# Performance work log

Measured on AMD Instinct MI355X. Metric: run time of the kernel, lower is better.

Reference implementation:

```python
import jax, jax.numpy as jnp
from jax import lax
import numpy as np

D_MODEL = 1024
EXP = 2
D_INNER = EXP * D_MODEL
D_STATE = 16
D_CONV = 4
DT_RANK = 64  # ceil(d_model/16), mamba default
NUM_GROUPS = 4
BSZ, SEQ = 2, 2048
EPS = 1e-5


def setup_inputs() -> dict:
    key = jax.random.key(0)
    ks = jax.random.split(key, 10)
    def n(k, shape, s=0.02):
        return jax.random.normal(k, shape, jnp.float32) * s
    return dict(
        x=jax.random.normal(ks[0], (BSZ, SEQ, D_MODEL), jnp.float32),
        ln1_g=jnp.ones((D_MODEL,), jnp.float32), ln1_b=jnp.zeros((D_MODEL,), jnp.float32),
        ln2_g=jnp.ones((D_MODEL,), jnp.float32), ln2_b=jnp.zeros((D_MODEL,), jnp.float32),
        W1=n(ks[1], (EXP * D_MODEL, D_MODEL)), b1=jnp.zeros((EXP * D_MODEL,), jnp.float32),
        W2=n(ks[2], (D_MODEL, EXP * D_MODEL)), b2=jnp.zeros((D_MODEL,), jnp.float32),
        in_proj_w=n(ks[3], (2 * D_INNER, D_MODEL)),
        conv_w=n(ks[4], (D_INNER, 1, D_CONV), 0.2), conv_b=jnp.zeros((D_INNER,), jnp.float32),
        x_proj_w=n(ks[5], (DT_RANK + 2 * D_STATE, D_INNER)),
        dt_proj_w=n(ks[6], (D_INNER, DT_RANK), 0.1), dt_proj_b=n(ks[7], (D_INNER,), 0.5),
        A_log=jnp.tile(jnp.log(jnp.arange(1, D_STATE + 1, dtype=jnp.float32)), (D_INNER, 1)),
        D_param=jnp.ones((D_INNER,), jnp.float32),
        out_proj_w=n(ks[8], (D_MODEL, D_INNER)),
    )


def _layernorm(x, g, b):
    m = jnp.mean(x, -1, keepdims=True)
    v = jnp.var(x, -1, keepdims=True)
    return (x - m) * lax.rsqrt(v + EPS) * g + b


def _ste_sign(w):
    # sign quantization with straight-through estimator (groupwise split is a no-op for sign)
    return w + lax.stop_gradient(jnp.sign(w) - w)


def _quant_act_groupwise(x, b=8):
    # groups along seq dim (x.shape[1]); gamma is the abs-max over the whole group slab
    Qb = float(2 ** (b - 1))
    B_, L, D = x.shape
    g = x.reshape(B_, NUM_GROUPS, L // NUM_GROUPS, D)
    gamma = jnp.max(jnp.abs(g), axis=(0, 2, 3), keepdims=True)
    q = jnp.clip(g * Qb / (gamma + EPS), -Qb + EPS, Qb - EPS)
    return q.reshape(B_, L, D)


def _mamba(u, in_proj_w, conv_w, conv_b, x_proj_w, dt_proj_w, dt_proj_b, A_log, D_param, out_proj_w):
    B_, L, _ = u.shape
    xz = u @ in_proj_w.T                         # [B, L, 2*d_inner]
    xs, z = jnp.split(xz, 2, axis=-1)
    # depthwise causal conv1d
    xt = jnp.transpose(xs, (0, 2, 1))            # [B, d_inner, L]
    xt = lax.conv_general_dilated(xt, conv_w, (1,), [(D_CONV - 1, 0)],
                                  feature_group_count=D_INNER,
                                  dimension_numbers=('NCH', 'OIH', 'NCH'))
    xt = xt + conv_b[None, :, None]
    xs = jax.nn.silu(jnp.transpose(xt, (0, 2, 1)))  # [B, L, d_inner]
    x_dbl = xs @ x_proj_w.T                      # [B, L, dt_rank + 2*d_state]
    dt, Bm, Cm = jnp.split(x_dbl, [DT_RANK, DT_RANK + D_STATE], axis=-1)
    dt = jax.nn.softplus(dt @ dt_proj_w.T + dt_proj_b)   # [B, L, d_inner]
    A = -jnp.exp(A_log)                          # [d_inner, d_state]

    def step(h, inp):
        dt_s, B_s, C_s, x_s = inp                # [B,di], [B,ds], [B,ds], [B,di]
        dA = jnp.exp(dt_s[..., None] * A)        # [B, di, ds]
        h = h * dA + (dt_s * x_s)[..., None] * B_s[:, None, :]
        y = jnp.einsum('bds,bs->bd', h, C_s)
        return h, y

    tm = lambda a: jnp.transpose(a, (1, 0, 2))   # time-major
    h0 = jnp.zeros((B_, D_INNER, D_STATE), u.dtype)
    _, ys = lax.scan(step, h0, (tm(dt), tm(Bm), tm(Cm), tm(xs)))
    y = jnp.transpose(ys, (1, 0, 2)) + D_param * xs
    y = y * jax.nn.silu(z)
    return y @ out_proj_w.T


def reference(x, ln1_g, ln1_b, ln2_g, ln2_b, W1, b1, W2, b2,
              in_proj_w, conv_w, conv_b, x_proj_w, dt_proj_w, dt_proj_b,
              A_log, D_param, out_proj_w):
    qW1 = _ste_sign(W1)
    qW2 = _ste_sign(W2)
    gated = jnp.clip(_layernorm(x, ln1_g, ln1_b) @ qW1.T + b1, -1.0, 1.0)  # Hardtanh
    x = x + gated @ qW2.T + b2
    qx = _quant_act_groupwise(x)
    out = qx + _mamba(_layernorm(qx, ln2_g, ln2_b), in_proj_w, conv_w, conv_b,
                      x_proj_w, dt_proj_w, dt_proj_b, A_log, D_param, out_proj_w)
    return out
```

## Files before the change

kernel.cpp:

```cpp
#include <hip/hip_runtime.h>
#include <math.h>

#define D_MODEL 1024
#define D_INNER 2048
#define D_STATE 16
#define DT_RANK 64
#define BSZ 2
#define SEQ 2048
#define NTOK (BSZ*SEQ)
#define NCH  (BSZ*D_INNER)
#define NCHUNK 64
#define CLEN 32
#define EPS 1e-5f

typedef __attribute__((ext_vector_type(8))) short short8v;
typedef __attribute__((ext_vector_type(4))) float f32x4;

__device__ __forceinline__ float sgnf(float w) {
    return (w > 0.f) ? 1.f : ((w < 0.f) ? -1.f : 0.f);
}
__device__ __forceinline__ unsigned short f2bf(float f) {
    unsigned int x = __float_as_uint(f);
    x += 0x7fffu + ((x >> 16) & 1u);
    return (unsigned short)(x >> 16);
}
__device__ __forceinline__ float bf2f(unsigned short u) {
    return __uint_as_float(((unsigned int)u) << 16);
}
__device__ __forceinline__ void stage16(const unsigned short* g, unsigned short* l) {
    __builtin_amdgcn_global_load_lds(
        (const __attribute__((address_space(1))) unsigned int*)g,
        (__attribute__((address_space(3))) unsigned int*)l, 16, 0, 0);
}

#define F4_W1   524288
#define F4_C1   524288
#define F4_C2   1048576
#define F4_C3   2097152
#define F4_C4   2146304
#define F4_C5   2179072
#define F4_C6   2703360
__global__ __launch_bounds__(256) void f2bf_all_kernel(
    const float* __restrict__ W1, const float* __restrict__ W2,
    const float* __restrict__ inpj, const float* __restrict__ xpj,
    const float* __restrict__ dtpj, const float* __restrict__ outpj,
    unsigned short* __restrict__ o_w1, unsigned short* __restrict__ o_w2,
    unsigned short* __restrict__ o_in, unsigned short* __restrict__ o_xp,
    unsigned short* __restrict__ o_dt, unsigned short* __restrict__ o_out)
{
    int i = blockIdx.x * 256 + threadIdx.x;
    if (i >= F4_C6) return;
    const float* src; unsigned short* dst; int off; bool sign = false;
    if (i < F4_C1)      { src = W1;   dst = o_w1;  off = i;          sign = true; }
    else if (i < F4_C2) { src = W2;   dst = o_w2;  off = i - F4_C1;  sign = true; }
    else if (i < F4_C3) { src = inpj; dst = o_in;  off = i - F4_C2; }
    else if (i < F4_C4) { src = xpj;  dst = o_xp;  off = i - F4_C3; }
    else if (i < F4_C5) { src = dtpj; dst = o_dt;  off = i - F4_C4; }
    else                { src = outpj;dst = o_out; off = i - F4_C5; }
    float4 v = reinterpret_cast<const float4*>(src)[off];
    if (sign) { v.x = sgnf(v.x); v.y = sgnf(v.y); v.z = sgnf(v.z); v.w = sgnf(v.w); }
    ushort4 o;
    o.x = f2bf(v.x); o.y = f2bf(v.y); o.z = f2bf(v.z); o.w = f2bf(v.w);
    reinterpret_cast<ushort4*>(dst)[off] = o;
}

__global__ __launch_bounds__(256) void ln_hilo_kernel(const float* __restrict__ x,
                                                      const float* __restrict__ g,
                                                      const float* __restrict__ b,
                                                      unsigned short* __restrict__ hi,
                                                      unsigned short* __restrict__ lo) {
    int row = blockIdx.x, tid = threadIdx.x;
    float4 v = reinterpret_cast<const float4*>(x + (size_t)row * D_MODEL)[tid];
    float s = v.x + v.y + v.z + v.w;
    float q = v.x*v.x + v.y*v.y + v.z*v.z + v.w*v.w;
    #pragma unroll
    for (int off = 32; off > 0; off >>= 1) { s += __shfl_down(s, off); q += __shfl_down(q, off); }
    __shared__ float rs[4], rq[4], smean, srstd;
    if ((tid & 63) == 0) { rs[tid >> 6] = s; rq[tid >> 6] = q; }
    __syncthreads();
    if (tid == 0) {
        float ts = rs[0]+rs[1]+rs[2]+rs[3], tq = rq[0]+rq[1]+rq[2]+rq[3];
        float mean = ts * (1.0f / D_MODEL);
        smean = mean;
        srstd = rsqrtf(tq * (1.0f / D_MODEL) - mean*mean + EPS);
    }
    __syncthreads();
    float mean = smean, rstd = srstd;
    float4 gg = reinterpret_cast<const float4*>(g)[tid];
    float4 bb = reinterpret_cast<const float4*>(b)[tid];
    float o[4];
    o[0] = (v.x-mean)*rstd*gg.x + bb.x; o[1] = (v.y-mean)*rstd*gg.y + bb.y;
    o[2] = (v.z-mean)*rstd*gg.z + bb.z; o[3] = (v.w-mean)*rstd*gg.w + bb.w;
    ushort4 h4, l4;
    h4.x = f2bf(o[0]); l4.x = f2bf(o[0] - bf2f(h4.x));
    h4.y = f2bf(o[1]); l4.y = f2bf(o[1] - bf2f(h4.y));
    h4.z = f2bf(o[2]); l4.z = f2bf(o[2] - bf2f(h4.z));
    h4.w = f2bf(o[3]); l4.w = f2bf(o[3] - bf2f(h4.w));
    reinterpret_cast<ushort4*>(hi + (size_t)row * D_MODEL)[tid] = h4;
    reinterpret_cast<ushort4*>(lo + (size_t)row * D_MODEL)[tid] = l4;
}

template<int EP, bool DUALA>
__global__ __launch_bounds__(256) void mfma_gemm(
    const unsigned short* __restrict__ A, const unsigned short* __restrict__ A2,
    const unsigned short* __restrict__ B, float* __restrict__ C,
    unsigned short* __restrict__ Cb,
    int M, int N, int K, int sA, int sC,
    const float* __restrict__ bias, const float* __restrict__ addx, int sAdd,
    unsigned int* __restrict__ gma)
{
    __shared__ __align__(16) unsigned short As[128*32];
    __shared__ __align__(16) unsigned short As2[DUALA ? 128*32 : 8];
    __shared__ __align__(16) unsigned short Bs[128*32];
    __shared__ float redmax[4];
    const int tid = threadIdx.x;
    const int lane = tid & 63;
    const int w = tid >> 6;
    const int wm = w >> 1, wn = w & 1;
    const int row0 = blockIdx.y * 128, col0 = blockIdx.x * 128;
    const int srow = lane >> 2;
    const int scol = (lane & 3) * 8;

    f32x4 acc[4][4];
    #pragma unroll
    for (int m = 0; m < 4; ++m)
        #pragma unroll
        for (int n = 0; n < 4; ++n)
            acc[m][n] = (f32x4){0.f, 0.f, 0.f, 0.f};

    for (int k0 = 0; k0 < K; k0 += 32) {
        #pragma unroll
        for (int i = 0; i < 2; ++i) {
            const int rbase = w * 32 + i * 16;
            stage16(A + (size_t)(row0 + rbase + srow) * sA + k0 + scol, &As[rbase * 32]);
            if (DUALA)
                stage16(A2 + (size_t)(row0 + rbase + srow) * sA + k0 + scol, &As2[rbase * 32]);
            if (col0 + rbase < N)
                stage16(B + (size_t)(col0 + rbase + srow) * K + k0 + scol, &Bs[rbase * 32]);
        }
        __syncthreads();

        short8v af[4], bfr[4], af2[4];
        const int fr = lane & 15, kg = (lane >> 4) * 8;
        #pragma unroll
        for (int m = 0; m < 4; ++m)
            af[m] = *reinterpret_cast<const short8v*>(&As[(wm*64 + m*16 + fr) * 32 + kg]);
        if (DUALA) {
            #pragma unroll
            for (int m = 0; m < 4; ++m)
                af2[m] = *reinterpret_cast<const short8v*>(&As2[(wm*64 + m*16 + fr) * 32 + kg]);
        }
        #pragma unroll
        for (int n = 0; n < 4; ++n)
            bfr[n] = *reinterpret_cast<const short8v*>(&Bs[(wn*64 + n*16 + fr) * 32 + kg]);

        #pragma unroll
        for (int m = 0; m < 4; ++m)
            #pragma unroll
            for (int n = 0; n < 4; ++n) {
                acc[m][n] = __builtin_amdgcn_mfma_f32_16x16x32_bf16(af[m], bfr[n], acc[m][n], 0, 0, 0);
                if (DUALA)
                    acc[m][n] = __builtin_amdgcn_mfma_f32_16x16x32_bf16(af2[m], bfr[n], acc[m][n], 0, 0, 0);
            }
        __syncthreads();
    }

    const int fc = lane & 15, r4 = (lane >> 4) * 4;
    float lmax = 0.0f;
    #pragma unroll
    for (int m = 0; m < 4; ++m) {
        const int grb = row0 + wm*64 + m*16 + r4;
        #pragma unroll
        for (int n = 0; n < 4; ++n) {
            const int gc = col0 + wn*64 + n*16 + fc;
            if (gc >= N) continue;
            #pragma unroll
            for (int j = 0; j < 4; ++j) {
                const int r = grb + j;
                float v = acc[m][n][j];
                if (EP == 0) {
                    C[(size_t)r*sC + gc] = v;
                } else if (EP == 1) {
                    v += bias[gc];
                    v = fminf(1.0f, fmaxf(-1.0f, v));
                    Cb[(size_t)r*sC + gc] = f2bf(v);
                } else if (EP == 3) {
                    float t = v + bias[gc];
                    C[(size_t)r*sC + gc] = fmaxf(t, 0.0f) + log1pf(__expf(-fabsf(t)));
                } else if (EP == 4) {
                    C[(size_t)r*sC + gc] = v + addx[(size_t)r*sAdd + gc];
                } else if (EP == 5) {
                    C[(size_t)r*sC + gc] = v;
                    if (gc < 64) Cb[(size_t)r*64 + gc] = f2bf(v);
                } else if (EP == 6) {
                    Cb[(size_t)r*sC + gc] = f2bf(v);
                } else {
                    v += bias[gc] + addx[(size_t)r*sAdd + gc];
                    C[(size_t)r*sC + gc] = v;
                    lmax = fmaxf(lmax, fabsf(v));
                }
            }
        }
    }
    if (EP == 7) {
        #pragma unroll
        for (int off = 32; off > 0; off >>= 1) lmax = fmaxf(lmax, __shfl_down(lmax, off));
        if (lane == 0) redmax[w] = lmax;
        __syncthreads();
        if (tid == 0) {
            float t = fmaxf(fmaxf(redmax[0], redmax[1]), fmaxf(redmax[2], redmax[3]));
            int g = (row0 & (SEQ - 1)) >> 9;
            atomicMax(gma + g, __float_as_uint(t));
        }
    }
}

__global__ __launch_bounds__(64) void init_gamma_kernel(unsigned int* g) {
    if (threadIdx.x < 4) g[threadIdx.x] = 0u;
}

__global__ __launch_bounds__(256) void quant_ln_kernel(
    const float* __restrict__ x2, const unsigned int* __restrict__ gamma_bits,
    const float* __restrict__ g, const float* __restrict__ b,
    float* __restrict__ qx, unsigned short* __restrict__ u)
{
    int row = blockIdx.x, tid = threadIdx.x;
    int grp = (row & (SEQ - 1)) >> 9;
    float gamma = __uint_as_float(gamma_bits[grp]);
    float scale = 128.0f / (gamma + EPS);
    const float lo = -128.0f + EPS, hi = 128.0f - EPS;
    float4 v = reinterpret_cast<const float4*>(x2 + (size_t)row * D_MODEL)[tid];
    float4 qv;
    qv.x = fminf(hi, fmaxf(lo, v.x * scale));
    qv.y = fminf(hi, fmaxf(lo, v.y * scale));
    qv.z = fminf(hi, fmaxf(lo, v.z * scale));
    qv.w = fminf(hi, fmaxf(lo, v.w * scale));
    reinterpret_cast<float4*>(qx + (size_t)row * D_MODEL)[tid] = qv;
    float s = qv.x + qv.y + qv.z + qv.w;
    float q = qv.x*qv.x + qv.y*qv.y + qv.z*qv.z + qv.w*qv.w;
    #pragma unroll
    for (int off = 32; off > 0; off >>= 1) { s += __shfl_down(s, off); q += __shfl_down(q, off); }
    __shared__ float rs[4], rq[4], smean, srstd;
    if ((tid & 63) == 0) { rs[tid >> 6] = s; rq[tid >> 6] = q; }
    __syncthreads();
    if (tid == 0) {
        float ts = rs[0]+rs[1]+rs[2]+rs[3], tq = rq[0]+rq[1]+rq[2]+rq[3];
        float mean = ts * (1.0f / D_MODEL);
        smean = mean;
        srstd = rsqrtf(tq * (1.0f / D_MODEL) - mean*mean + EPS);
    }
    __syncthreads();
    float mean = smean, rstd = srstd;
    float4 gg = reinterpret_cast<const float4*>(g)[tid];
    float4 bb = reinterpret_cast<const float4*>(b)[tid];
    ushort4 o;
    o.x = f2bf((qv.x-mean)*rstd*gg.x + bb.x);
    o.y = f2bf((qv.y-mean)*rstd*gg.y + bb.y);
    o.z = f2bf((qv.z-mean)*rstd*gg.z + bb.z);
    o.w = f2bf((qv.w-mean)*rstd*gg.w + bb.w);
    reinterpret_cast<ushort4*>(u + (size_t)row * D_MODEL)[tid] = o;
}

__global__ __launch_bounds__(256) void conv_silu_kernel(const unsigned short* __restrict__ xz,
                                                        const float* __restrict__ conv_w,
                                                        const float* __restrict__ conv_b,
                                                        unsigned short* __restrict__ xcb) {
    int c = blockIdx.x * 256 + threadIdx.x;
    int m = blockIdx.y;
    int b = m >> 11, l = m & (SEQ - 1);
    float4 w4 = reinterpret_cast<const float4*>(conv_w)[c];
    float wv[4] = {w4.x, w4.y, w4.z, w4.w};
    float s = conv_b[c];
    const unsigned short* base = xz + ((size_t)b * SEQ) * 4096 + c;
    #pragma unroll
    for (int k = 0; k < 4; ++k) {
        int ll = l - 3 + k;
        if (ll >= 0) s += bf2f(base[(size_t)ll * 4096]) * wv[k];
    }
    float sig = 1.0f / (1.0f + __expf(-s));
    xcb[(size_t)m * D_INNER + c] = f2bf(s * sig);
}

__device__ __forceinline__ void make_dA(float dA[D_STATE], float dtv,
                                        const float* a, bool pw) {
    if (pw) {
        dA[0] = __expf(dtv * a[0]);
        #pragma unroll
        for (int s = 1; s < D_STATE; ++s) dA[s] = dA[s>>1] * dA[(s-1)>>1];
    } else {
        #pragma unroll
        for (int s = 0; s < D_STATE; ++s) dA[s] = __expf(dtv * a[s]);
    }
}

__global__ __launch_bounds__(256) void scan_partial_kernel(
    const float* __restrict__ dt, const unsigned short* __restrict__ xcb,
    const float* __restrict__ xdbl, const float* __restrict__ A_log,
    float* __restrict__ Lbuf, float* __restrict__ Sbuf)
{
    int gtid = blockIdx.x * 256 + threadIdx.x;
    int ch = gtid & (NCH - 1);
    int c  = gtid >> 12;
    int b = ch >> 11, d = ch & (D_INNER - 1);
    float a[D_STATE], h[D_STATE];
    bool pw = true;
    #pragma unroll
    for (int s = 0; s < D_STATE; ++s) {
        a[s] = -__expf(A_log[(size_t)d * D_STATE + s]);
        h[s] = 0.0f;
    }
    #pragma unroll
    for (int s = 1; s < D_STATE; ++s)
        pw = pw && (fabsf(a[s] - a[0]*(float)(s+1)) <= 1e-3f * fabsf(a[s]));

    size_t m0 = (size_t)b * SEQ + (size_t)c * CLEN;
    float Ssum = 0.0f;

    float dt_n = dt[m0 * D_INNER + d];
    float x_n  = bf2f(xcb[m0 * D_INNER + d]);
    float4 B_n[4];
    {
        const float* xd = xdbl + m0 * 96;
        #pragma unroll
        for (int i = 0; i < 4; ++i)
            B_n[i] = *reinterpret_cast<const float4*>(xd + DT_RANK + 4*i);
    }

    for (int l = 0; l < CLEN; ++l) {
        float dtv = dt_n, xv = x_n;
        float Bc[D_STATE];
        #pragma unroll
        for (int i = 0; i < 4; ++i) {
            Bc[4*i+0] = B_n[i].x; Bc[4*i+1] = B_n[i].y; Bc[4*i+2] = B_n[i].z; Bc[4*i+3] = B_n[i].w;
        }
        if (l + 1 < CLEN) {
            size_t m1 = m0 + l + 1;
            dt_n = dt[m1 * D_INNER + d];
            x_n  = bf2f(xcb[m1 * D_INNER + d]);
            const float* xd = xdbl + m1 * 96;
            #pragma unroll
            for (int i = 0; i < 4; ++i)
                B_n[i] = *reinterpret_cast<const float4*>(xd + DT_RANK + 4*i);
        }
        Ssum += dtv;
        float dx = dtv * xv;
        float dA[D_STATE];
        make_dA(dA, dtv, a, pw);
        #pragma unroll
        for (int s = 0; s < D_STATE; ++s)
            h[s] = h[s] * dA[s] + dx * Bc[s];
    }
    float4* Lp = reinterpret_cast<float4*>(Lbuf + (size_t)c * (NCH * D_STATE) + (size_t)ch * D_STATE);
    Lp[0] = make_float4(h[0], h[1], h[2], h[3]);
    Lp[1] = make_float4(h[4], h[5], h[6], h[7]);
    Lp[2] = make_float4(h[8], h[9], h[10], h[11]);
    Lp[3] = make_float4(h[12], h[13], h[14], h[15]);
    Sbuf[(size_t)c * NCH + ch] = Ssum;
}

__global__ __launch_bounds__(256) void scan_combine_kernel(
    float* __restrict__ LH, const float* __restrict__ Sbuf,
    const float* __restrict__ A_log)
{
    int gtid = blockIdx.x * 256 + threadIdx.x;
    int s = gtid & (D_STATE - 1);
    int ch = gtid >> 4;
    int d = ch & (D_INNER - 1);
    float a = -__expf(A_log[(size_t)d * D_STATE + s]);
    float h = 0.0f;
    #pragma unroll 4
    for (int c = 0; c < NCHUNK; ++c) {
        size_t idx = (size_t)c * (NCH * D_STATE) + (size_t)ch * D_STATE + s;
        float loc = LH[idx];
        LH[idx] = h;
        float P = __expf(a * Sbuf[(size_t)c * NCH + ch]);
        h = h * P + loc;
    }
}

__global__ __launch_bounds__(256) void scan_final_kernel(
    const float* __restrict__ dt, const unsigned short* __restrict__ xcb,
    const unsigned short* __restrict__ xzb, const float* __restrict__ xdbl,
    const float* __restrict__ A_log, const float* __restrict__ D_param,
    const float* __restrict__ Hin, unsigned short* __restrict__ yb)
{
    int gtid = blockIdx.x * 256 + threadIdx.x;
    int ch = gtid & (NCH - 1);
    int c  = gtid >> 12;
    int b = ch >> 11, d = ch & (D_INNER - 1);
    float a[D_STATE], h[D_STATE];
    {
        const float4* Hp = reinterpret_cast<const float4*>(
            Hin + (size_t)c * (NCH * D_STATE) + (size_t)ch * D_STATE);
        float4 h0 = Hp[0], h1 = Hp[1], h2 = Hp[2], h3 = Hp[3];
        h[0]=h0.x; h[1]=h0.y; h[2]=h0.z; h[3]=h0.w;
        h[4]=h1.x; h[5]=h1.y; h[6]=h1.z; h[7]=h1.w;
        h[8]=h2.x; h[9]=h2.y; h[10]=h2.z; h[11]=h2.w;
        h[12]=h3.x; h[13]=h3.y; h[14]=h3.z; h[15]=h3.w;
    }
    bool pw = true;
    #pragma unroll
    for (int s = 0; s < D_STATE; ++s)
        a[s] = -__expf(A_log[(size_t)d * D_STATE + s]);
    #pragma unroll
    for (int s = 1; s < D_STATE; ++s)
        pw = pw && (fabsf(a[s] - a[0]*(float)(s+1)) <= 1e-3f * fabsf(a[s]));
    float Dp = D_param[d];

    size_t m0 = (size_t)b * SEQ + (size_t)c * CLEN;
    float dt_n = dt[m0 * D_INNER + d];
    float x_n  = bf2f(xcb[m0 * D_INNER + d]);
    float z_n  = bf2f(xzb[m0 * 4096 + D_INNER + d]);
    float4 B_n[4], C_n[4];
    {
        const float* xd = xdbl + m0 * 96;
        #pragma unroll
        for (int i = 0; i < 4; ++i) {
            B_n[i] = *reinterpret_cast<const float4*>(xd + DT_RANK + 4*i);
            C_n[i] = *reinterpret_cast<const float4*>(xd + DT_RANK + D_STATE + 4*i);
        }
    }

    for (int l = 0; l < CLEN; ++l) {
        float dtv = dt_n, xv = x_n, zv = z_n;
        float Bc[D_STATE], Cc[D_STATE];
        #pragma unroll
        for (int i = 0; i < 4; ++i) {
            Bc[4*i+0] = B_n[i].x; Bc[4*i+1] = B_n[i].y; Bc[4*i+2] = B_n[i].z; Bc[4*i+3] = B_n[i].w;
            Cc[4*i+0] = C_n[i].x; Cc[4*i+1] = C_n[i].y; Cc[4*i+2] = C_n[i].z; Cc[4*i+3] = C_n[i].w;
        }
        if (l + 1 < CLEN) {
            size_t m1 = m0 + l + 1;
            dt_n = dt[m1 * D_INNER + d];
            x_n  = bf2f(xcb[m1 * D_INNER + d]);
            z_n  = bf2f(xzb[m1 * 4096 + D_INNER + d]);
            const float* xd = xdbl + m1 * 96;
            #pragma unroll
            for (int i = 0; i < 4; ++i) {
                B_n[i] = *reinterpret_cast<const float4*>(xd + DT_RANK + 4*i);
                C_n[i] = *reinterpret_cast<const float4*>(xd + DT_RANK + D_STATE + 4*i);
            }
        }
        float dx = dtv * xv;
        float yv = 0.0f;
        float dA[D_STATE];
        make_dA(dA, dtv, a, pw);
        #pragma unroll
        for (int s = 0; s < D_STATE; ++s) {
            h[s] = h[s] * dA[s] + dx * Bc[s];
            yv += h[s] * Cc[s];
        }
        yv += Dp * xv;
        float sig = 1.0f / (1.0f + __expf(-zv));
        yb[(m0 + l) * D_INNER + d] = f2bf(yv * (zv * sig));
    }
}

extern "C" void kernel_launch(void* const* d_in, const int* in_sizes, int n_in,
                              void* d_out, int out_size, void* d_ws, size_t ws_size,
                              hipStream_t stream) {
    const float* x         = (const float*)d_in[0];
    const float* ln1_g     = (const float*)d_in[1];
    const float* ln1_b     = (const float*)d_in[2];
    const float* ln2_g     = (const float*)d_in[3];
    const float* ln2_b     = (const float*)d_in[4];
    const float* W1        = (const float*)d_in[5];
    const float* b1        = (const float*)d_in[6];
    const float* W2        = (const float*)d_in[7];
    const float* b2        = (const float*)d_in[8];
    const float* in_proj   = (const float*)d_in[9];
    const float* conv_w    = (const float*)d_in[10];
    const float* conv_b    = (const float*)d_in[11];
    const float* x_proj    = (const float*)d_in[12];
    const float* dt_proj   = (const float*)d_in[13];
    const float* dt_proj_b = (const float*)d_in[14];
    const float* A_log     = (const float*)d_in[15];
    const float* D_param   = (const float*)d_in[16];
    const float* out_proj  = (const float*)d_in[17];
    float* out = (float*)d_out;

    char* ws = (char*)d_ws;
    float*          f_x2   = (float*)         (ws + 0);
    unsigned short* b_xz   = (unsigned short*)(ws + 16777216);
    float*          f_dt   = (float*)         (ws + 50331648);
    float*          f_xdbl = (float*)         (ws + 83886080);
    float*          f_L    = (float*)         (ws + 85458944);
    float*          f_S    = (float*)         (ws + 102236160);
    unsigned int*   f_gamma= (unsigned int*)  (ws + 103284736);
    unsigned short* b_a1hi = (unsigned short*)(ws + 103284800);
    unsigned short* b_a1lo = b_a1hi + 4194304;
    unsigned short* b_y    = b_a1hi;
    unsigned short* b_gated= (unsigned short*)(ws + 120062016);
    unsigned short* b_xc   = b_gated;
    unsigned short* b_u    = (unsigned short*)(ws + 136839232);
    unsigned short* b_xdt  = b_u;
    unsigned short* b_w1s  = (unsigned short*)(ws + 145227840);
    unsigned short* b_w2s  = (unsigned short*)(ws + 149422144);
    unsigned short* b_inpj = (unsigned short*)(ws + 153616448);
    unsigned short* b_xpj  = (unsigned short*)(ws + 162005056);
    unsigned short* b_dtpj = (unsigned short*)(ws + 162398272);
    unsigned short* b_outpj= (unsigned short*)(ws + 162660416);

    dim3 b256(256);

    f2bf_all_kernel<<<dim3((F4_C6 + 255)/256), b256, 0, stream>>>(
        W1, W2, in_proj, x_proj, dt_proj, out_proj,
        b_w1s, b_w2s, b_inpj, b_xpj, b_dtpj, b_outpj);

    ln_hilo_kernel<<<dim3(NTOK), b256, 0, stream>>>(x, ln1_g, ln1_b, b_a1hi, b_a1lo);
    mfma_gemm<1, true><<<dim3(16, 32), b256, 0, stream>>>(
        b_a1hi, b_a1lo, b_w1s, nullptr, b_gated, NTOK, D_INNER, D_MODEL, D_MODEL, D_INNER,
        b1, nullptr, 0, nullptr);
    init_gamma_kernel<<<1, 64, 0, stream>>>(f_gamma);
    mfma_gemm<7, false><<<dim3(8, 32), b256, 0, stream>>>(
        b_gated, nullptr, b_w2s, f_x2, nullptr, NTOK, D_MODEL, D_INNER, D_INNER, D_MODEL,
        b2, x, D_MODEL, f_gamma);
    quant_ln_kernel<<<dim3(NTOK), b256, 0, stream>>>(f_x2, f_gamma, ln2_g, ln2_b, f_x2, b_u);
    mfma_gemm<6, false><<<dim3(32, 32), b256, 0, stream>>>(
        b_u, nullptr, b_inpj, nullptr, b_xz, NTOK, 2*D_INNER, D_MODEL, D_MODEL, 2*D_INNER,
        nullptr, nullptr, 0, nullptr);
    conv_silu_kernel<<<dim3(D_INNER/256, NTOK), b256, 0, stream>>>(b_xz, conv_w, conv_b, b_xc);
    mfma_gemm<5, false><<<dim3(1, 32), b256, 0, stream>>>(
        b_xc, nullptr, b_xpj, f_xdbl, b_xdt, NTOK, DT_RANK + 2*D_STATE, D_INNER, D_INNER,
        DT_RANK + 2*D_STATE, nullptr, nullptr, 0, nullptr);
    mfma_gemm<3, false><<<dim3(16, 32), b256, 0, stream>>>(
        b_xdt, nullptr, b_dtpj, f_dt, nullptr, NTOK, D_INNER, DT_RANK, DT_RANK, D_INNER,
        dt_proj_b, nullptr, 0, nullptr);
    scan_partial_kernel<<<dim3(NCH*NCHUNK/256), b256, 0, stream>>>(
        f_dt, b_xc, f_xdbl, A_log, f_L, f_S);
    scan_combine_kernel<<<dim3(NCH*D_STATE/256), b256, 0, stream>>>(f_L, f_S, A_log);
    scan_final_kernel<<<dim3(NCH*NCHUNK/256), b256, 0, stream>>>(
        f_dt, b_xc, b_xz, f_xdbl, A_log, D_param, f_L, b_y);
    mfma_gemm<4, false><<<dim3(8, 32), b256, 0, stream>>>(
        b_y, nullptr, b_outpj, out, nullptr, NTOK, D_MODEL, D_INNER, D_INNER, D_MODEL,
        nullptr, f_x2, D_MODEL, nullptr);
}
```

Before: 502.0 us.

## Add narrow N tiles and split-K x_proj GEMM to raise block counts

The GEMM template gains a BN parameter, so several GEMMs run with 64-wide N tiles and launch twice as many blocks on the many-CU GPU. The tiny x_proj GEMM, which previously launched only 32 blocks, is split four ways along K into partial buffers, and a new combine kernel sums them and writes the bf16 dt slice. The gamma init launch is folded into the weight-conversion kernel. In exchange, the 64-wide tiles reuse less of each A tile from LDS, and split-K adds an extra kernel launch and partial-buffer traffic.

```diff
diff --git a/kernel.cpp b/kernel.cpp
--- a/kernel.cpp
+++ b/kernel.cpp
@@ -33,7 +33,6 @@
         (__attribute__((address_space(3))) unsigned int*)l, 16, 0, 0);
 }
 
-#define F4_W1   524288
 #define F4_C1   524288
 #define F4_C2   1048576
 #define F4_C3   2097152
@@ -46,9 +45,11 @@
     const float* __restrict__ dtpj, const float* __restrict__ outpj,
     unsigned short* __restrict__ o_w1, unsigned short* __restrict__ o_w2,
     unsigned short* __restrict__ o_in, unsigned short* __restrict__ o_xp,
-    unsigned short* __restrict__ o_dt, unsigned short* __restrict__ o_out)
+    unsigned short* __restrict__ o_dt, unsigned short* __restrict__ o_out,
+    unsigned int* __restrict__ gma)
 {
     int i = blockIdx.x * 256 + threadIdx.x;
+    if (blockIdx.x == 0 && threadIdx.x < 4) gma[threadIdx.x] = 0u;
     if (i >= F4_C6) return;
     const float* src; unsigned short* dst; int off; bool sign = false;
     if (i < F4_C1)      { src = W1;   dst = o_w1;  off = i;          sign = true; }
@@ -100,47 +101,59 @@
     reinterpret_cast<ushort4*>(lo + (size_t)row * D_MODEL)[tid] = l4;
 }
 
-template<int EP, bool DUALA>
+template<int EP, bool DUALA, int BN, bool KSPLIT>
 __global__ __launch_bounds__(256) void mfma_gemm(
     const unsigned short* __restrict__ A, const unsigned short* __restrict__ A2,
     const unsigned short* __restrict__ B, float* __restrict__ C,
     unsigned short* __restrict__ Cb,
     int M, int N, int K, int sA, int sC,
     const float* __restrict__ bias, const float* __restrict__ addx, int sAdd,
-    unsigned int* __restrict__ gma)
-{
+    unsigned int* __restrict__ gma, int ksl)
+{
+    constexpr int NF = BN / 32;
     __shared__ __align__(16) unsigned short As[128*32];
     __shared__ __align__(16) unsigned short As2[DUALA ? 128*32 : 8];
-    __shared__ __align__(16) unsigned short Bs[128*32];
+    __shared__ __align__(16) unsigned short Bs[BN*32];
     __shared__ float redmax[4];
     const int tid = threadIdx.x;
     const int lane = tid & 63;
     const int w = tid >> 6;
     const int wm = w >> 1, wn = w & 1;
-    const int row0 = blockIdx.y * 128, col0 = blockIdx.x * 128;
+    const int row0 = blockIdx.y * 128, col0 = blockIdx.x * BN;
     const int srow = lane >> 2;
     const int scol = (lane & 3) * 8;
 
-    f32x4 acc[4][4];
+    int k_begin = 0, k_end = K;
+    if (KSPLIT) {
+        int z = blockIdx.z;
+        k_begin = z * ksl; k_end = k_begin + ksl;
+        C += (size_t)z * M * sC;
+    }
+
+    f32x4 acc[4][NF];
     #pragma unroll
     for (int m = 0; m < 4; ++m)
         #pragma unroll
-        for (int n = 0; n < 4; ++n)
+        for (int n = 0; n < NF; ++n)
             acc[m][n] = (f32x4){0.f, 0.f, 0.f, 0.f};
 
-    for (int k0 = 0; k0 < K; k0 += 32) {
+    for (int k0 = k_begin; k0 < k_end; k0 += 32) {
         #pragma unroll
         for (int i = 0; i < 2; ++i) {
             const int rbase = w * 32 + i * 16;
             stage16(A + (size_t)(row0 + rbase + srow) * sA + k0 + scol, &As[rbase * 32]);
             if (DUALA)
                 stage16(A2 + (size_t)(row0 + rbase + srow) * sA + k0 + scol, &As2[rbase * 32]);
+        }
+        #pragma unroll
+        for (int i = 0; i < BN/64; ++i) {
+            const int rbase = (BN == 128) ? (w * 32 + i * 16) : (w * 16);
             if (col0 + rbase < N)
                 stage16(B + (size_t)(col0 + rbase + srow) * K + k0 + scol, &Bs[rbase * 32]);
         }
         __syncthreads();
 
-        short8v af[4], bfr[4], af2[4];
+        short8v af[4], bfr[NF], af2[4];
         const int fr = lane & 15, kg = (lane >> 4) * 8;
         #pragma unroll
         for (int m = 0; m < 4; ++m)
@@ -151,13 +164,13 @@
                 af2[m] = *reinterpret_cast<const short8v*>(&As2[(wm*64 + m*16 + fr) * 32 + kg]);
         }
         #pragma unroll
-        for (int n = 0; n < 4; ++n)
-            bfr[n] = *reinterpret_cast<const short8v*>(&Bs[(wn*64 + n*16 + fr) * 32 + kg]);
+        for (int n = 0; n < NF; ++n)
+            bfr[n] = *reinterpret_cast<const short8v*>(&Bs[(wn*(BN/2) + n*16 + fr) * 32 + kg]);
 
         #pragma unroll
         for (int m = 0; m < 4; ++m)
             #pragma unroll
-            for (int n = 0; n < 4; ++n) {
+            for (int n = 0; n < NF; ++n) {
                 acc[m][n] = __builtin_amdgcn_mfma_f32_16x16x32_bf16(af[m], bfr[n], acc[m][n], 0, 0, 0);
                 if (DUALA)
                     acc[m][n] = __builtin_amdgcn_mfma_f32_16x16x32_bf16(af2[m], bfr[n], acc[m][n], 0, 0, 0);
@@ -171,8 +184,8 @@
     for (int m = 0; m < 4; ++m) {
         const int grb = row0 + wm*64 + m*16 + r4;
         #pragma unroll
-        for (int n = 0; n < 4; ++n) {
-            const int gc = col0 + wn*64 + n*16 + fc;
+        for (int n = 0; n < NF; ++n) {
+            const int gc = col0 + wn*(BN/2) + n*16 + fc;
             if (gc >= N) continue;
             #pragma unroll
             for (int j = 0; j < 4; ++j) {
@@ -189,9 +202,6 @@
                     C[(size_t)r*sC + gc] = fmaxf(t, 0.0f) + log1pf(__expf(-fabsf(t)));
                 } else if (EP == 4) {
                     C[(size_t)r*sC + gc] = v + addx[(size_t)r*sAdd + gc];
-                } else if (EP == 5) {
-                    C[(size_t)r*sC + gc] = v;
-                    if (gc < 64) Cb[(size_t)r*64 + gc] = f2bf(v);
                 } else if (EP == 6) {
                     Cb[(size_t)r*sC + gc] = f2bf(v);
                 } else {
@@ -215,8 +225,30 @@
     }
 }
 
-__global__ __launch_bounds__(64) void init_gamma_kernel(unsigned int* g) {
-    if (threadIdx.x < 4) g[threadIdx.x] = 0u;
+__global__ __launch_bounds__(256) void xproj_combine_kernel(
+    const float* __restrict__ part,
+    float* __restrict__ xdbl,
+    unsigned short* __restrict__ xdt)
+{
+    int i = blockIdx.x * 256 + threadIdx.x;
+    if (i >= NTOK * 24) return;
+    const size_t stride = (size_t)NTOK * 96 / 4;
+    float4 v0 = reinterpret_cast<const float4*>(part)[i];
+    float4 v1 = reinterpret_cast<const float4*>(part)[i + stride];
+    float4 v2 = reinterpret_cast<const float4*>(part)[i + 2*stride];
+    float4 v3 = reinterpret_cast<const float4*>(part)[i + 3*stride];
+    float4 o;
+    o.x = (v0.x + v1.x) + (v2.x + v3.x);
+    o.y = (v0.y + v1.y) + (v2.y + v3.y);
+    o.z = (v0.z + v1.z) + (v2.z + v3.z);
+    o.w = (v0.w + v1.w) + (v2.w + v3.w);
+    reinterpret_cast<float4*>(xdbl)[i] = o;
+    int row = i / 24, c4 = i % 24;
+    if (c4 < 16) {
+        ushort4 u;
+        u.x = f2bf(o.x); u.y = f2bf(o.y); u.z = f2bf(o.z); u.w = f2bf(o.w);
+        reinterpret_cast<ushort4*>(xdt + (size_t)row * 64)[c4] = u;
+    }
 }
 
 __global__ __launch_bounds__(256) void quant_ln_kernel(
@@ -485,6 +517,7 @@
     float*          f_dt   = (float*)         (ws + 50331648);
     float*          f_xdbl = (float*)         (ws + 83886080);
     float*          f_L    = (float*)         (ws + 85458944);
+    float*          f_xp   = f_L;
     float*          f_S    = (float*)         (ws + 102236160);
     unsigned int*   f_gamma= (unsigned int*)  (ws + 103284736);
     unsigned short* b_a1hi = (unsigned short*)(ws + 103284800);
@@ -505,33 +538,33 @@
 
     f2bf_all_kernel<<<dim3((F4_C6 + 255)/256), b256, 0, stream>>>(
         W1, W2, in_proj, x_proj, dt_proj, out_proj,
-        b_w1s, b_w2s, b_inpj, b_xpj, b_dtpj, b_outpj);
+        b_w1s, b_w2s, b_inpj, b_xpj, b_dtpj, b_outpj, f_gamma);
 
     ln_hilo_kernel<<<dim3(NTOK), b256, 0, stream>>>(x, ln1_g, ln1_b, b_a1hi, b_a1lo);
-    mfma_gemm<1, true><<<dim3(16, 32), b256, 0, stream>>>(
+    mfma_gemm<1, true, 64, false><<<dim3(32, 32), b256, 0, stream>>>(
         b_a1hi, b_a1lo, b_w1s, nullptr, b_gated, NTOK, D_INNER, D_MODEL, D_MODEL, D_INNER,
-        b1, nullptr, 0, nullptr);
-    init_gamma_kernel<<<1, 64, 0, stream>>>(f_gamma);
-    mfma_gemm<7, false><<<dim3(8, 32), b256, 0, stream>>>(
+        b1, nullptr, 0, nullptr, 0);
+    mfma_gemm<7, false, 64, false><<<dim3(16, 32), b256, 0, stream>>>(
         b_gated, nullptr, b_w2s, f_x2, nullptr, NTOK, D_MODEL, D_INNER, D_INNER, D_MODEL,
-        b2, x, D_MODEL, f_gamma);
+        b2, x, D_MODEL, f_gamma, 0);
     quant_ln_kernel<<<dim3(NTOK), b256, 0, stream>>>(f_x2, f_gamma, ln2_g, ln2_b, f_x2, b_u);
-    mfma_gemm<6, false><<<dim3(32, 32), b256, 0, stream>>>(
+    mfma_gemm<6, false, 128, false><<<dim3(32, 32), b256, 0, stream>>>(
         b_u, nullptr, b_inpj, nullptr, b_xz, NTOK, 2*D_INNER, D_MODEL, D_MODEL, 2*D_INNER,
-        nullptr, nullptr, 0, nullptr);
+        nullptr, nullptr, 0, nullptr, 0);
     conv_silu_kernel<<<dim3(D_INNER/256, NTOK), b256, 0, stream>>>(b_xz, conv_w, conv_b, b_xc);
-    mfma_gemm<5, false><<<dim3(1, 32), b256, 0, stream>>>(
-        b_xc, nullptr, b_xpj, f_xdbl, b_xdt, NTOK, DT_RANK + 2*D_STATE, D_INNER, D_INNER,
-        DT_RANK + 2*D_STATE, nullptr, nullptr, 0, nullptr);
-    mfma_gemm<3, false><<<dim3(16, 32), b256, 0, stream>>>(
+    mfma_gemm<0, false, 128, true><<<dim3(1, 32, 4), b256, 0, stream>>>(
+        b_xc, nullptr, b_xpj, f_xp, nullptr, NTOK, DT_RANK + 2*D_STATE, D_INNER, D_INNER,
+        DT_RANK + 2*D_STATE, nullptr, nullptr, 0, nullptr, 512);
+    xproj_combine_kernel<<<dim3((NTOK*24 + 255)/256), b256, 0, stream>>>(f_xp, f_xdbl, b_xdt);
+    mfma_gemm<3, false, 64, false><<<dim3(32, 32), b256, 0, stream>>>(
         b_xdt, nullptr, b_dtpj, f_dt, nullptr, NTOK, D_INNER, DT_RANK, DT_RANK, D_INNER,
-        dt_proj_b, nullptr, 0, nullptr);
+        dt_proj_b, nullptr, 0, nullptr, 0);
     scan_partial_kernel<<<dim3(NCH*NCHUNK/256), b256, 0, stream>>>(
         f_dt, b_xc, f_xdbl, A_log, f_L, f_S);
     scan_combine_kernel<<<dim3(NCH*D_STATE/256), b256, 0, stream>>>(f_L, f_S, A_log);
     scan_final_kernel<<<dim3(NCH*NCHUNK/256), b256, 0, stream>>>(
         f_dt, b_xc, b_xz, f_xdbl, A_log, D_param, f_L, b_y);
-    mfma_gemm<4, false><<<dim3(8, 32), b256, 0, stream>>>(
+    mfma_gemm<4, false, 64, false><<<dim3(16, 32), b256, 0, stream>>>(
         b_y, nullptr, b_outpj, out, nullptr, NTOK, D_MODEL, D_INNER, D_INNER, D_MODEL,
-        nullptr, f_x2, D_MODEL, nullptr);
-}
+        nullptr, f_x2, D_MODEL, nullptr, 0);
+}
```

After: 478.2 us. 4.7% less time.
